# Optimization experiments

Measured on AMD Instinct MI355X. Metric: run time of the kernel, lower is better.

The kernel has to match this reference:

```python
import jax, jax.numpy as jnp
import numpy as np

BN_EPS = 1e-5
N_NODES = 100000
N_EDGES = 1600000
IN_DIM = 128
HID = 256   # 2 * out_dim
OUT_DIM = 128


def setup_inputs() -> dict:
    key = jax.random.key(0)
    ks = jax.random.split(key, 8)
    x = jax.random.normal(ks[0], (N_NODES, IN_DIM), dtype=jnp.float32)
    edge_index = jax.random.randint(ks[1], (2, N_EDGES), 0, N_NODES, dtype=jnp.int32)
    # GINConv learned eps (train_eps=True), init 0
    eps = jnp.zeros((), dtype=jnp.float32)
    # MLP: Linear(in, 2*out) -> BN -> ReLU -> Linear(2*out, out)
    s1 = 1.0 / np.sqrt(IN_DIM)
    s2 = 1.0 / np.sqrt(HID)
    W1 = jax.random.uniform(ks[2], (IN_DIM, HID), jnp.float32, -s1, s1)
    b1 = jax.random.uniform(ks[3], (HID,), jnp.float32, -s1, s1)
    g1 = jnp.ones((HID,), jnp.float32)
    beta1 = jnp.zeros((HID,), jnp.float32)
    W2 = jax.random.uniform(ks[4], (HID, OUT_DIM), jnp.float32, -s2, s2)
    b2 = jax.random.uniform(ks[5], (OUT_DIM,), jnp.float32, -s2, s2)
    # outer BatchNorm
    g2 = jnp.ones((OUT_DIM,), jnp.float32)
    beta2 = jnp.zeros((OUT_DIM,), jnp.float32)
    return {"x": x, "edge_index": edge_index, "eps": eps,
            "W1": W1, "b1": b1, "g1": g1, "beta1": beta1,
            "W2": W2, "b2": b2, "g2": g2, "beta2": beta2}


def _batchnorm(h, gamma, beta):
    # training-mode BatchNorm1d: batch mean, biased variance
    mu = jnp.mean(h, axis=0)
    var = jnp.mean(jnp.square(h - mu), axis=0)
    return (h - mu) * jax.lax.rsqrt(var + BN_EPS) * gamma + beta


def reference(x, edge_index, eps, W1, b1, g1, beta1, W2, b2, g2, beta2):
    src, dst = edge_index[0], edge_index[1]
    # sum-aggregation of neighbor features: scatter-add x[src] onto dst
    aggr = jax.ops.segment_sum(x[src], dst, num_segments=x.shape[0])  # [N, in_dim]
    h = (1.0 + eps) * x + aggr
    # MLP: Linear -> BN -> ReLU -> Linear
    h = h @ W1 + b1
    h = jax.nn.relu(_batchnorm(h, g1, beta1))
    h = h @ W2 + b2
    # outer BN + ReLU
    return jax.nn.relu(_batchnorm(h, g2, beta2))
```

## Files before the change

kernel.cpp:

```cpp
#include <hip/hip_runtime.h>
#include <hip/hip_bf16.h>

#define N_NODES 100000
#define N_EDGES 1600000
#define IN_DIM  128
#define HID     256
#define OUT_DIM 128
#define BN_EPS  1e-5f

typedef unsigned int u32;
typedef unsigned short u16;
typedef __attribute__((ext_vector_type(8))) short short8v;
typedef __attribute__((ext_vector_type(4))) float f32x4;

__device__ __forceinline__ float bf2f(u16 h) {
    return __uint_as_float(((u32)h) << 16);
}
__device__ __forceinline__ u16 f2bf(float f) {
    u32 u = __float_as_uint(f);
    u32 r = (u + 0x7fffu + ((u >> 16) & 1u)) >> 16;
    return (u16)r;
}
__device__ __forceinline__ u32 pack2(float a, float b) {
    return (u32)f2bf(a) | ((u32)f2bf(b) << 16);
}
__device__ __forceinline__ void gload16(const void* g, void* l) {
    __builtin_amdgcn_global_load_lds((const __attribute__((address_space(1))) u32*)g,
                                     (__attribute__((address_space(3))) u32*)l, 16, 0, 0);
}
#define MFMA(a,b,c) __builtin_amdgcn_mfma_f32_16x16x32_bf16(a, b, c, 0, 0, 0)

__global__ __launch_bounds__(256) void k_prepx(const float* __restrict__ x,
                                               uint2* __restrict__ xb) {
    int i = blockIdx.x * 256 + threadIdx.x;
    const int total = N_NODES * 32;
    if (i < total) {
        float4 v = ((const float4*)x)[i];
        uint2 p;
        p.x = pack2(v.x, v.y);
        p.y = pack2(v.z, v.w);
        xb[i] = p;
    }
}

__global__ __launch_bounds__(256) void k_link(const int* __restrict__ ei,
                                              int* __restrict__ head,
                                              int2* __restrict__ nxt) {
    int e = blockIdx.x * 256 + threadIdx.x;
    if (e >= N_EDGES) return;
    int dst = ei[N_EDGES + e];
    int src = ei[e];
    int old = atomicExch(&head[dst], e);
    nxt[e] = make_int2(old, src);
}

__global__ __launch_bounds__(256) void k_aggregate(const uint2* __restrict__ xb,
                                                   const int2* __restrict__ nxt,
                                                   const int* __restrict__ head,
                                                   const float* __restrict__ epsp,
                                                   char* __restrict__ aggrb) {
    int node = blockIdx.x * 8 + (threadIdx.x >> 5);
    int l = threadIdx.x & 31;
    uint2 s = xb[node * 32 + l];
    float sc = 1.0f + epsp[0];
    float a0 = bf2f((u16)s.x) * sc, a1 = bf2f((u16)(s.x >> 16)) * sc;
    float a2 = bf2f((u16)s.y) * sc, a3 = bf2f((u16)(s.y >> 16)) * sc;
    int e = head[node];
    while (e >= 0) {
        int2 nv = nxt[e];
        int src = nv.y;
        e = nv.x;
        uint2 v = xb[src * 32 + l];
        a0 += bf2f((u16)v.x); a1 += bf2f((u16)(v.x >> 16));
        a2 += bf2f((u16)v.y); a3 += bf2f((u16)(v.y >> 16));
    }
    u32 b = ((u32)node * 256 + (u32)l * 8) ^ (((u32)(node & 7)) << 4);
    uint2 p; p.x = pack2(a0, a1); p.y = pack2(a2, a3);
    *(uint2*)(aggrb + b) = p;
}

__global__ __launch_bounds__(256) void k_prepw(const float* __restrict__ W1,
                                               const float* __restrict__ W2,
                                               char* __restrict__ w1t,
                                               char* __restrict__ w2t) {
    int t = blockIdx.x * 256 + threadIdx.x;
    u16 tmp[8];
    if (t < 4096) {
        int j = t >> 4, kc = t & 15;
        #pragma unroll
        for (int i = 0; i < 8; ++i) tmp[i] = f2bf(W1[(kc * 8 + i) * HID + j]);
        u32 off = ((u32)(j * 256 + kc * 16)) ^ (((u32)(j & 7)) << 4);
        uint4 q;
        q.x = (u32)tmp[0] | ((u32)tmp[1] << 16);
        q.y = (u32)tmp[2] | ((u32)tmp[3] << 16);
        q.z = (u32)tmp[4] | ((u32)tmp[5] << 16);
        q.w = (u32)tmp[6] | ((u32)tmp[7] << 16);
        *(uint4*)(w1t + off) = q;
    } else {
        int t2 = t - 4096;
        int j = t2 >> 5, kc = t2 & 31;
        #pragma unroll
        for (int i = 0; i < 8; ++i) tmp[i] = f2bf(W2[(kc * 8 + i) * OUT_DIM + j]);
        u32 off = ((u32)(j * 512 + kc * 16)) ^ (((u32)(j & 7)) << 4);
        uint4 q;
        q.x = (u32)tmp[0] | ((u32)tmp[1] << 16);
        q.y = (u32)tmp[2] | ((u32)tmp[3] << 16);
        q.z = (u32)tmp[4] | ((u32)tmp[5] << 16);
        q.w = (u32)tmp[6] | ((u32)tmp[7] << 16);
        *(uint4*)(w2t + off) = q;
    }
}

__global__ __launch_bounds__(512) void k_gemm1(const char* __restrict__ aggrb,
                                               const char* __restrict__ w1t,
                                               const float* __restrict__ b1,
                                               u16* __restrict__ h1u,
                                               float* __restrict__ gstats) {
    __shared__ u16 Als[160 * 128];
    __shared__ u16 Bls[256 * 128];
    __shared__ float slds[512];

    const int tid = threadIdx.x, lane = tid & 63, w = tid >> 6;
    const int wr = w >> 2, wc = w & 3;
    const int base = blockIdx.x * 160;

    slds[tid] = 0.f;

    char* lA = (char*)Als;
    char* lB = (char*)Bls;
    const char* ga = aggrb + (size_t)base * 256;
    #pragma unroll
    for (int i = 0; i < 5; ++i)
        gload16(ga + i * 8192 + w * 1024 + (lane << 4), lA + i * 8192 + w * 1024);
    #pragma unroll
    for (int i = 0; i < 8; ++i)
        gload16(w1t + i * 8192 + w * 1024 + (lane << 4), lB + i * 8192 + w * 1024);

    const int rA = lane & 15;
    const int kb = (lane >> 4) << 3;
    const u32 xsw = ((u32)(rA & 7)) << 4;
    int colv[4]; float bcol[4];
    #pragma unroll
    for (int n = 0; n < 4; ++n) { colv[n] = wc * 64 + n * 16 + rA; bcol[n] = b1[colv[n]]; }

    asm volatile("s_waitcnt vmcnt(0)" ::: "memory");
    __syncthreads();

    f32x4 acc[5][4];
    #pragma unroll
    for (int m = 0; m < 5; ++m)
        #pragma unroll
        for (int n = 0; n < 4; ++n) acc[m][n] = (f32x4){0.f, 0.f, 0.f, 0.f};

    #pragma unroll
    for (int ks = 0; ks < 4; ++ks) {
        const int kk2 = (ks * 32 + kb) * 2;
        short8v a[5], b[4];
        #pragma unroll
        for (int m = 0; m < 5; ++m) {
            u32 off = ((u32)((wr * 80 + m * 16 + rA) * 256 + kk2)) ^ xsw;
            a[m] = *(const short8v*)(lA + off);
        }
        #pragma unroll
        for (int n = 0; n < 4; ++n) {
            u32 off = ((u32)(colv[n] * 256 + kk2)) ^ xsw;
            b[n] = *(const short8v*)(lB + off);
        }
        #pragma unroll
        for (int m = 0; m < 5; ++m)
            #pragma unroll
            for (int n = 0; n < 4; ++n)
                acc[m][n] = MFMA(a[m], b[n], acc[m][n]);
    }

    float csum[4] = {0.f,0.f,0.f,0.f}, csq[4] = {0.f,0.f,0.f,0.f};
    #pragma unroll
    for (int m = 0; m < 5; ++m) {
        int r0 = base + wr * 80 + m * 16 + ((lane >> 4) << 2);
        #pragma unroll
        for (int n = 0; n < 4; ++n) {
            f32x4 d = acc[m][n];
            #pragma unroll
            for (int r = 0; r < 4; ++r) {
                float v = d[r] + bcol[n];
                csum[n] += v; csq[n] += v * v;
                h1u[(size_t)(r0 + r) * 256 + colv[n]] = f2bf(v);
            }
        }
    }
    #pragma unroll
    for (int n = 0; n < 4; ++n) {
        csum[n] += __shfl_xor(csum[n], 16); csum[n] += __shfl_xor(csum[n], 32);
        csq[n]  += __shfl_xor(csq[n], 16);  csq[n]  += __shfl_xor(csq[n], 32);
    }
    if (lane < 16) {
        #pragma unroll
        for (int n = 0; n < 4; ++n) {
            atomicAdd(&slds[colv[n]], csum[n]);
            atomicAdd(&slds[256 + colv[n]], csq[n]);
        }
    }
    __syncthreads();
    atomicAdd(&gstats[tid], slds[tid]);
}

__global__ __launch_bounds__(512) void k_gemm2(const u16* __restrict__ h1u,
                                               const char* __restrict__ w2t,
                                               const float* __restrict__ b2,
                                               const float* __restrict__ g1,
                                               const float* __restrict__ beta1,
                                               const float* __restrict__ gstats,
                                               float* __restrict__ out,
                                               float* __restrict__ gstats2) {
    __shared__ u16 Als[160 * 128];
    __shared__ u16 Bls[128 * 256];
    __shared__ float a1s[256], b1s[256];
    __shared__ float slds[256];

    const int tid = threadIdx.x, lane = tid & 63, w = tid >> 6;
    const int wr = w >> 2, wc = w & 3;
    const int base = blockIdx.x * 160;

    if (tid < 256) {
        float s = gstats[tid], sq = gstats[256 + tid];
        float mu = s * (1.0f / N_NODES);
        float var = sq * (1.0f / N_NODES) - mu * mu;
        float inv = rsqrtf(var + BN_EPS);
        float a = g1[tid] * inv;
        a1s[tid] = a;
        b1s[tid] = beta1[tid] - mu * a;
        slds[tid] = 0.f;
    }

    char* lA = (char*)Als;
    char* lB = (char*)Bls;
    #pragma unroll
    for (int i = 0; i < 8; ++i)
        gload16(w2t + i * 8192 + w * 1024 + (lane << 4), lB + i * 8192 + w * 1024);

    const int rA = lane & 15;
    const int kb = (lane >> 4) << 3;
    const u32 xsw = ((u32)(rA & 7)) << 4;
    int colv[2]; float bcol[2];
    #pragma unroll
    for (int n = 0; n < 2; ++n) { colv[n] = wc * 32 + n * 16 + rA; bcol[n] = b2[colv[n]]; }

    __syncthreads();

    f32x4 acc[5][2];
    #pragma unroll
    for (int m = 0; m < 5; ++m)
        #pragma unroll
        for (int n = 0; n < 2; ++n) acc[m][n] = (f32x4){0.f, 0.f, 0.f, 0.f};

    for (int kh = 0; kh < 2; ++kh) {
        #pragma unroll
        for (int i = 0; i < 10; ++i) {
            int id = tid + i * 512;
            int r = id >> 5;
            int c = id & 31;
            uint2 v = *(const uint2*)(h1u + (size_t)(base + r) * 256 + kh * 128 + c * 4);
            int cg = kh * 128 + c * 4;
            float4 av = *(const float4*)&a1s[cg];
            float4 bv = *(const float4*)&b1s[cg];
            float f0 = fmaxf(bf2f((u16)v.x)         * av.x + bv.x, 0.f);
            float f1 = fmaxf(bf2f((u16)(v.x >> 16)) * av.y + bv.y, 0.f);
            float f2 = fmaxf(bf2f((u16)v.y)         * av.z + bv.z, 0.f);
            float f3 = fmaxf(bf2f((u16)(v.y >> 16)) * av.w + bv.w, 0.f);
            uint2 p; p.x = pack2(f0, f1); p.y = pack2(f2, f3);
            u32 off = ((u32)(r * 256 + c * 8)) ^ (((u32)(r & 7)) << 4);
            *(uint2*)(lA + off) = p;
        }
        if (kh == 0) asm volatile("s_waitcnt vmcnt(0)" ::: "memory");
        __syncthreads();

        #pragma unroll
        for (int ks = 0; ks < 4; ++ks) {
            const int kk2 = (ks * 32 + kb) * 2;
            short8v a[5], b[2];
            #pragma unroll
            for (int m = 0; m < 5; ++m) {
                u32 off = ((u32)((wr * 80 + m * 16 + rA) * 256 + kk2)) ^ xsw;
                a[m] = *(const short8v*)(lA + off);
            }
            #pragma unroll
            for (int n = 0; n < 2; ++n) {
                u32 off = ((u32)(colv[n] * 512 + kh * 256 + kk2)) ^ xsw;
                b[n] = *(const short8v*)(lB + off);
            }
            #pragma unroll
            for (int m = 0; m < 5; ++m)
                #pragma unroll
                for (int n = 0; n < 2; ++n)
                    acc[m][n] = MFMA(a[m], b[n], acc[m][n]);
        }
        __syncthreads();
    }

    float csum[2] = {0.f,0.f}, csq[2] = {0.f,0.f};
    #pragma unroll
    for (int m = 0; m < 5; ++m) {
        int r0 = base + wr * 80 + m * 16 + ((lane >> 4) << 2);
        #pragma unroll
        for (int n = 0; n < 2; ++n) {
            f32x4 d = acc[m][n];
            #pragma unroll
            for (int r = 0; r < 4; ++r) {
                float v = d[r] + bcol[n];
                csum[n] += v; csq[n] += v * v;
                out[(size_t)(r0 + r) * 128 + colv[n]] = v;
            }
        }
    }
    #pragma unroll
    for (int n = 0; n < 2; ++n) {
        csum[n] += __shfl_xor(csum[n], 16); csum[n] += __shfl_xor(csum[n], 32);
        csq[n]  += __shfl_xor(csq[n], 16);  csq[n]  += __shfl_xor(csq[n], 32);
    }
    if (lane < 16) {
        #pragma unroll
        for (int n = 0; n < 2; ++n) {
            atomicAdd(&slds[colv[n]], csum[n]);
            atomicAdd(&slds[128 + colv[n]], csq[n]);
        }
    }
    __syncthreads();
    if (tid < 256) atomicAdd(&gstats2[tid], slds[tid]);
}

__global__ __launch_bounds__(256) void k_bn2(float* __restrict__ out,
                                             const float* __restrict__ gstats2,
                                             const float* __restrict__ g2,
                                             const float* __restrict__ beta2) {
    int i = blockIdx.x * 256 + threadIdx.x;
    const int total = N_NODES * OUT_DIM / 4;
    if (i >= total) return;
    float4 v = ((float4*)out)[i];
    int c = (i & 31) * 4;
    float vv[4] = {v.x, v.y, v.z, v.w};
    float res[4];
    #pragma unroll
    for (int j = 0; j < 4; ++j) {
        float s = gstats2[c + j], sq = gstats2[OUT_DIM + c + j];
        float mu = s * (1.0f / N_NODES);
        float var = sq * (1.0f / N_NODES) - mu * mu;
        float inv = rsqrtf(var + BN_EPS);
        float a = g2[c + j] * inv;
        float b = beta2[c + j] - mu * a;
        res[j] = fmaxf(vv[j] * a + b, 0.f);
    }
    ((float4*)out)[i] = make_float4(res[0], res[1], res[2], res[3]);
}

extern "C" void kernel_launch(void* const* d_in, const int* in_sizes, int n_in,
                              void* d_out, int out_size, void* d_ws, size_t ws_size,
                              hipStream_t stream) {
    const float* x     = (const float*)d_in[0];
    const int*   ei    = (const int*)d_in[1];
    const float* epsp  = (const float*)d_in[2];
    const float* W1    = (const float*)d_in[3];
    const float* b1    = (const float*)d_in[4];
    const float* g1    = (const float*)d_in[5];
    const float* beta1 = (const float*)d_in[6];
    const float* W2    = (const float*)d_in[7];
    const float* b2    = (const float*)d_in[8];
    const float* g2    = (const float*)d_in[9];
    const float* beta2 = (const float*)d_in[10];

    char* ws = (char*)d_ws;
    char*  aggrb   = ws;
    u16*   h1u     = (u16*)(ws + 25600000);
    int2*  nxt     = (int2*)(ws + 25600000);
    int*   head    = (int*)(ws + 38400000);
    uint2* xb      = (uint2*)(ws + 40000000);
    float* gstats  = (float*)(ws + 76800000);
    float* gstats2 = gstats + 512;
    char*  w1t     = ws + 76804096;
    char*  w2t     = ws + 76869632;
    float* out = (float*)d_out;

    hipMemsetAsync(head, 0xFF, 400000, stream);
    hipMemsetAsync(gstats, 0, 768 * sizeof(float), stream);

    k_prepx<<<(N_NODES * 32 + 255) / 256, 256, 0, stream>>>(x, xb);
    k_link<<<(N_EDGES + 255) / 256, 256, 0, stream>>>(ei, head, nxt);
    k_prepw<<<32, 256, 0, stream>>>(W1, W2, w1t, w2t);
    k_aggregate<<<N_NODES / 8, 256, 0, stream>>>(xb, nxt, head, epsp, aggrb);
    k_gemm1<<<625, 512, 0, stream>>>(aggrb, w1t, b1, h1u, gstats);
    k_gemm2<<<625, 512, 0, stream>>>(h1u, w2t, b2, g1, beta1, gstats, out, gstats2);
    k_bn2<<<(N_NODES * OUT_DIM / 4 + 255) / 256, 256, 0, stream>>>(out, gstats2, g2, beta2);
}
```

Baseline: 282.3 us.

## Fuse prep kernels, split adjacency lists in two, store pre-BN output as bf16

Merges the x-to-bf16 conversion, edge linking and weight transposition into one launch. Each node's adjacency list is split into two chains, chosen by edge parity, so two 16-lane groups walk half the edges each with 16-byte loads and combine their sums with a shuffle; this shortens the serial pointer chase. The second GEMM now writes its pre-BN output as bf16 into workspace, and the final BN pass reads it and writes fp32, roughly halving that intermediate traffic. The cost is extra rounding of the pre-BN values and a larger head array to clear.

```diff
diff --git a/kernel.cpp b/kernel.cpp
--- a/kernel.cpp
+++ b/kernel.cpp
@@ -30,84 +30,101 @@
 }
 #define MFMA(a,b,c) __builtin_amdgcn_mfma_f32_16x16x32_bf16(a, b, c, 0, 0, 0)
 
-__global__ __launch_bounds__(256) void k_prepx(const float* __restrict__ x,
-                                               uint2* __restrict__ xb) {
-    int i = blockIdx.x * 256 + threadIdx.x;
-    const int total = N_NODES * 32;
-    if (i < total) {
-        float4 v = ((const float4*)x)[i];
+__global__ __launch_bounds__(256) void k_prep(const float* __restrict__ x,
+                                              const int* __restrict__ ei,
+                                              const float* __restrict__ W1,
+                                              const float* __restrict__ W2,
+                                              uint2* __restrict__ xb,
+                                              int* __restrict__ head2,
+                                              int2* __restrict__ nxt,
+                                              char* __restrict__ w1t,
+                                              char* __restrict__ w2t) {
+    int t = blockIdx.x * 256 + threadIdx.x;
+    {
+        float4 v = ((const float4*)x)[t];
         uint2 p;
         p.x = pack2(v.x, v.y);
         p.y = pack2(v.z, v.w);
-        xb[i] = p;
-    }
-}
-
-__global__ __launch_bounds__(256) void k_link(const int* __restrict__ ei,
-                                              int* __restrict__ head,
-                                              int2* __restrict__ nxt) {
-    int e = blockIdx.x * 256 + threadIdx.x;
-    if (e >= N_EDGES) return;
-    int dst = ei[N_EDGES + e];
-    int src = ei[e];
-    int old = atomicExch(&head[dst], e);
-    nxt[e] = make_int2(old, src);
-}
-
-__global__ __launch_bounds__(256) void k_aggregate(const uint2* __restrict__ xb,
+        xb[t] = p;
+    }
+    if (t < N_EDGES) {
+        int dst = ei[N_EDGES + t];
+        int src = ei[t];
+        int old = atomicExch(&head2[dst * 2 + (t & 1)], t);
+        nxt[t] = make_int2(old, src);
+    }
+    if (t < 8192) {
+        u16 tmp[8];
+        if (t < 4096) {
+            int j = t >> 4, kc = t & 15;
+            #pragma unroll
+            for (int i = 0; i < 8; ++i) tmp[i] = f2bf(W1[(kc * 8 + i) * HID + j]);
+            u32 off = ((u32)(j * 256 + kc * 16)) ^ (((u32)(j & 7)) << 4);
+            uint4 q;
+            q.x = (u32)tmp[0] | ((u32)tmp[1] << 16);
+            q.y = (u32)tmp[2] | ((u32)tmp[3] << 16);
+            q.z = (u32)tmp[4] | ((u32)tmp[5] << 16);
+            q.w = (u32)tmp[6] | ((u32)tmp[7] << 16);
+            *(uint4*)(w1t + off) = q;
+        } else {
+            int t2 = t - 4096;
+            int j = t2 >> 5, kc = t2 & 31;
+            #pragma unroll
+            for (int i = 0; i < 8; ++i) tmp[i] = f2bf(W2[(kc * 8 + i) * OUT_DIM + j]);
+            u32 off = ((u32)(j * 512 + kc * 16)) ^ (((u32)(j & 7)) << 4);
+            uint4 q;
+            q.x = (u32)tmp[0] | ((u32)tmp[1] << 16);
+            q.y = (u32)tmp[2] | ((u32)tmp[3] << 16);
+            q.z = (u32)tmp[4] | ((u32)tmp[5] << 16);
+            q.w = (u32)tmp[6] | ((u32)tmp[7] << 16);
+            *(uint4*)(w2t + off) = q;
+        }
+    }
+}
+
+__global__ __launch_bounds__(256) void k_aggregate(const uint4* __restrict__ xb4,
                                                    const int2* __restrict__ nxt,
-                                                   const int* __restrict__ head,
+                                                   const int* __restrict__ head2,
                                                    const float* __restrict__ epsp,
                                                    char* __restrict__ aggrb) {
-    int node = blockIdx.x * 8 + (threadIdx.x >> 5);
-    int l = threadIdx.x & 31;
-    uint2 s = xb[node * 32 + l];
-    float sc = 1.0f + epsp[0];
-    float a0 = bf2f((u16)s.x) * sc, a1 = bf2f((u16)(s.x >> 16)) * sc;
-    float a2 = bf2f((u16)s.y) * sc, a3 = bf2f((u16)(s.y >> 16)) * sc;
-    int e = head[node];
+    const int lane = threadIdx.x & 63;
+    const int w = threadIdx.x >> 6;
+    const int q = lane >> 4, l = lane & 15;
+    const int nq = q >> 1, p = q & 1;
+    const int node = blockIdx.x * 8 + w * 2 + nq;
+
+    float a[8];
+    #pragma unroll
+    for (int i = 0; i < 8; ++i) a[i] = 0.f;
+
+    if (p == 0) {
+        float sc = 1.0f + epsp[0];
+        uint4 v = xb4[node * 16 + l];
+        a[0] = bf2f((u16)v.x) * sc;  a[1] = bf2f((u16)(v.x >> 16)) * sc;
+        a[2] = bf2f((u16)v.y) * sc;  a[3] = bf2f((u16)(v.y >> 16)) * sc;
+        a[4] = bf2f((u16)v.z) * sc;  a[5] = bf2f((u16)(v.z >> 16)) * sc;
+        a[6] = bf2f((u16)v.w) * sc;  a[7] = bf2f((u16)(v.w >> 16)) * sc;
+    }
+    int e = head2[node * 2 + p];
     while (e >= 0) {
         int2 nv = nxt[e];
-        int src = nv.y;
         e = nv.x;
-        uint2 v = xb[src * 32 + l];
-        a0 += bf2f((u16)v.x); a1 += bf2f((u16)(v.x >> 16));
-        a2 += bf2f((u16)v.y); a3 += bf2f((u16)(v.y >> 16));
-    }
-    u32 b = ((u32)node * 256 + (u32)l * 8) ^ (((u32)(node & 7)) << 4);
-    uint2 p; p.x = pack2(a0, a1); p.y = pack2(a2, a3);
-    *(uint2*)(aggrb + b) = p;
-}
-
-__global__ __launch_bounds__(256) void k_prepw(const float* __restrict__ W1,
-                                               const float* __restrict__ W2,
-                                               char* __restrict__ w1t,
-                                               char* __restrict__ w2t) {
-    int t = blockIdx.x * 256 + threadIdx.x;
-    u16 tmp[8];
-    if (t < 4096) {
-        int j = t >> 4, kc = t & 15;
-        #pragma unroll
-        for (int i = 0; i < 8; ++i) tmp[i] = f2bf(W1[(kc * 8 + i) * HID + j]);
-        u32 off = ((u32)(j * 256 + kc * 16)) ^ (((u32)(j & 7)) << 4);
-        uint4 q;
-        q.x = (u32)tmp[0] | ((u32)tmp[1] << 16);
-        q.y = (u32)tmp[2] | ((u32)tmp[3] << 16);
-        q.z = (u32)tmp[4] | ((u32)tmp[5] << 16);
-        q.w = (u32)tmp[6] | ((u32)tmp[7] << 16);
-        *(uint4*)(w1t + off) = q;
-    } else {
-        int t2 = t - 4096;
-        int j = t2 >> 5, kc = t2 & 31;
-        #pragma unroll
-        for (int i = 0; i < 8; ++i) tmp[i] = f2bf(W2[(kc * 8 + i) * OUT_DIM + j]);
-        u32 off = ((u32)(j * 512 + kc * 16)) ^ (((u32)(j & 7)) << 4);
-        uint4 q;
-        q.x = (u32)tmp[0] | ((u32)tmp[1] << 16);
-        q.y = (u32)tmp[2] | ((u32)tmp[3] << 16);
-        q.z = (u32)tmp[4] | ((u32)tmp[5] << 16);
-        q.w = (u32)tmp[6] | ((u32)tmp[7] << 16);
-        *(uint4*)(w2t + off) = q;
+        uint4 v = xb4[nv.y * 16 + l];
+        a[0] += bf2f((u16)v.x);  a[1] += bf2f((u16)(v.x >> 16));
+        a[2] += bf2f((u16)v.y);  a[3] += bf2f((u16)(v.y >> 16));
+        a[4] += bf2f((u16)v.z);  a[5] += bf2f((u16)(v.z >> 16));
+        a[6] += bf2f((u16)v.w);  a[7] += bf2f((u16)(v.w >> 16));
+    }
+    #pragma unroll
+    for (int i = 0; i < 8; ++i) a[i] += __shfl_xor(a[i], 16);
+    if (p == 0) {
+        uint4 o;
+        o.x = pack2(a[0], a[1]);
+        o.y = pack2(a[2], a[3]);
+        o.z = pack2(a[4], a[5]);
+        o.w = pack2(a[6], a[7]);
+        u32 b = ((u32)node * 256 + (u32)l * 16) ^ (((u32)(node & 7)) << 4);
+        *(uint4*)(aggrb + b) = o;
     }
 }
 
@@ -210,7 +227,7 @@
                                                const float* __restrict__ g1,
                                                const float* __restrict__ beta1,
                                                const float* __restrict__ gstats,
-                                               float* __restrict__ out,
+                                               u16* __restrict__ h2b,
                                                float* __restrict__ gstats2) {
     __shared__ u16 Als[160 * 128];
     __shared__ u16 Bls[128 * 256];
@@ -308,7 +325,7 @@
             for (int r = 0; r < 4; ++r) {
                 float v = d[r] + bcol[n];
                 csum[n] += v; csq[n] += v * v;
-                out[(size_t)(r0 + r) * 128 + colv[n]] = v;
+                h2b[(size_t)(r0 + r) * 128 + colv[n]] = f2bf(v);
             }
         }
     }
@@ -328,28 +345,32 @@
     if (tid < 256) atomicAdd(&gstats2[tid], slds[tid]);
 }
 
-__global__ __launch_bounds__(256) void k_bn2(float* __restrict__ out,
+__global__ __launch_bounds__(256) void k_bn2(const uint4* __restrict__ h2b4,
+                                             float* __restrict__ out,
                                              const float* __restrict__ gstats2,
                                              const float* __restrict__ g2,
                                              const float* __restrict__ beta2) {
     int i = blockIdx.x * 256 + threadIdx.x;
-    const int total = N_NODES * OUT_DIM / 4;
+    const int total = N_NODES * 16;
     if (i >= total) return;
-    float4 v = ((float4*)out)[i];
-    int c = (i & 31) * 4;
-    float vv[4] = {v.x, v.y, v.z, v.w};
-    float res[4];
-    #pragma unroll
-    for (int j = 0; j < 4; ++j) {
-        float s = gstats2[c + j], sq = gstats2[OUT_DIM + c + j];
+    uint4 v = h2b4[i];
+    int c0 = (i & 15) * 8;
+    u16 hv[8] = {(u16)v.x, (u16)(v.x >> 16), (u16)v.y, (u16)(v.y >> 16),
+                 (u16)v.z, (u16)(v.z >> 16), (u16)v.w, (u16)(v.w >> 16)};
+    float res[8];
+    #pragma unroll
+    for (int j = 0; j < 8; ++j) {
+        int c = c0 + j;
+        float s = gstats2[c], sq = gstats2[OUT_DIM + c];
         float mu = s * (1.0f / N_NODES);
         float var = sq * (1.0f / N_NODES) - mu * mu;
         float inv = rsqrtf(var + BN_EPS);
-        float a = g2[c + j] * inv;
-        float b = beta2[c + j] - mu * a;
-        res[j] = fmaxf(vv[j] * a + b, 0.f);
-    }
-    ((float4*)out)[i] = make_float4(res[0], res[1], res[2], res[3]);
+        float a = g2[c] * inv;
+        float b = beta2[c] - mu * a;
+        res[j] = fmaxf(bf2f(hv[j]) * a + b, 0.f);
+    }
+    ((float4*)out)[i * 2]     = make_float4(res[0], res[1], res[2], res[3]);
+    ((float4*)out)[i * 2 + 1] = make_float4(res[4], res[5], res[6], res[7]);
 }
 
 extern "C" void kernel_launch(void* const* d_in, const int* in_sizes, int n_in,
@@ -369,24 +390,23 @@
 
     char* ws = (char*)d_ws;
     char*  aggrb   = ws;
+    u16*   h2b     = (u16*)ws;
     u16*   h1u     = (u16*)(ws + 25600000);
     int2*  nxt     = (int2*)(ws + 25600000);
-    int*   head    = (int*)(ws + 38400000);
-    uint2* xb      = (uint2*)(ws + 40000000);
+    int*   head2   = (int*)(ws + 38400000);
+    uint2* xb      = (uint2*)(ws + 39200000);
     float* gstats  = (float*)(ws + 76800000);
     float* gstats2 = gstats + 512;
     char*  w1t     = ws + 76804096;
     char*  w2t     = ws + 76869632;
     float* out = (float*)d_out;
 
-    hipMemsetAsync(head, 0xFF, 400000, stream);
+    hipMemsetAsync(head2, 0xFF, 800000, stream);
     hipMemsetAsync(gstats, 0, 768 * sizeof(float), stream);
 
-    k_prepx<<<(N_NODES * 32 + 255) / 256, 256, 0, stream>>>(x, xb);
-    k_link<<<(N_EDGES + 255) / 256, 256, 0, stream>>>(ei, head, nxt);
-    k_prepw<<<32, 256, 0, stream>>>(W1, W2, w1t, w2t);
-    k_aggregate<<<N_NODES / 8, 256, 0, stream>>>(xb, nxt, head, epsp, aggrb);
+    k_prep<<<12500, 256, 0, stream>>>(x, ei, W1, W2, xb, head2, nxt, w1t, w2t);
+    k_aggregate<<<N_NODES / 8, 256, 0, stream>>>((const uint4*)xb, nxt, head2, epsp, aggrb);
     k_gemm1<<<625, 512, 0, stream>>>(aggrb, w1t, b1, h1u, gstats);
-    k_gemm2<<<625, 512, 0, stream>>>(h1u, w2t, b2, g1, beta1, gstats, out, gstats2);
-    k_bn2<<<(N_NODES * OUT_DIM / 4 + 255) / 256, 256, 0, stream>>>(out, gstats2, g2, beta2);
-}
+    k_gemm2<<<625, 512, 0, stream>>>(h1u, w2t, b2, g1, beta1, gstats, h2b, gstats2);
+    k_bn2<<<(N_NODES * 16 + 255) / 256, 256, 0, stream>>>((const uint4*)h2b, out, gstats2, g2, beta2);
+}
```

After: 259.1 us. -8.2%, faster.
